# Kernel optimization log

Measured on AMD Instinct MI355X. Metric: run time of the kernel, lower is better.

Reference implementation:

```python
import jax, jax.numpy as jnp
import numpy as np

# Model dims (match init_kwargs)
B, H_HIST, L, C = 2, 7, 256, 512
H = H_HIST + 1          # dialogue turns after concatenating current utterance
N_HEADS = 8
N_TOP = 4               # window_size
D_HEAD = C // N_HEADS


def setup_inputs() -> dict:
    key = jax.random.key(0)
    ks = jax.random.split(key, 12)
    s = 0.02
    return {
        "global_attn_map": jax.random.normal(ks[0], (B, H, H), jnp.float32),
        "history_context": jax.random.normal(ks[1], (B, H_HIST, L, C), jnp.float32),
        "current_context": jax.random.normal(ks[2], (B, L, C), jnp.float32),
        "h_context_mask": jnp.ones((B, H_HIST, L), jnp.bool_),
        "c_context_mask": jnp.ones((B, L), jnp.bool_),
        "history_mask": jnp.ones((B, H_HIST), jnp.bool_),
        # 3 experts stacked on leading axis: 0=self, 1=past, 2=future
        "Wq": s * jax.random.normal(ks[3], (3, C, C), jnp.float32),
        "bq": jnp.zeros((3, C), jnp.float32),
        "Wk": s * jax.random.normal(ks[4], (3, C, C), jnp.float32),
        "bk": jnp.zeros((3, C), jnp.float32),
        "Wv": s * jax.random.normal(ks[5], (3, C, C), jnp.float32),
        "bv": jnp.zeros((3, C), jnp.float32),
        "Wo": s * jax.random.normal(ks[6], (3, C, C), jnp.float32),
        "bo": jnp.zeros((3, C), jnp.float32),
    }


def _mha(ctx, indx, Wq, bq, Wk, bk, Wv, bv, Wo, bo):
    """Cross-attention of every turn j (query) against its top-k gathered turns (key/value).
    ctx: (b,H,l,c), indx: (b,H,K) indices into the turn axis. Returns (b,H,K,l,c)."""
    b, Ht, l, c = ctx.shape
    K = indx.shape[-1]
    scale = 1.0 / np.sqrt(D_HEAD)
    q = (ctx @ Wq + bq).reshape(b, Ht, l, N_HEADS, D_HEAD)
    k = (ctx @ Wk + bk).reshape(b, Ht, l, N_HEADS, D_HEAD)
    v = (ctx @ Wv + bv).reshape(b, Ht, l, N_HEADS, D_HEAD)
    bidx = jnp.arange(b)[:, None, None]
    kg = k[bidx, indx]          # (b,H,K,l,nh,d)  gather KV turns
    vg = v[bidx, indx]
    scores = jnp.einsum('bhind,bhkjnd->bhknij', q, kg) * scale   # (b,H,K,nh,l,l)
    attn = jax.nn.softmax(scores, axis=-1)
    out = jnp.einsum('bhknij,bhkjnd->bhkind', attn, vg).reshape(b, Ht, K, l, c)
    return out @ Wo + bo


def _wise(ctx, attn_map, indx, Wq, bq, Wk, bk, Wv, bv, Wo, bo):
    """Vectorized form of the triple python loop: for each (batch, turn j, slot k) pick
    self/past/future expert by comparing j with indx[b,j,k], then combine weighted by attn_map."""
    outs = [_mha(ctx, indx, Wq[e], bq[e], Wk[e], bk[e], Wv[e], bv[e], Wo[e], bo[e])
            for e in range(3)]  # each (b,H,K,l,c); 0=self,1=past,2=future
    j = jnp.arange(ctx.shape[1])[None, :, None]
    sel_self = (indx == j)[..., None, None]
    sel_future = (indx > j)[..., None, None]
    combined = jnp.where(sel_self, outs[0], jnp.where(sel_future, outs[2], outs[1]))
    return jnp.einsum('bhk,bhklc->bhlc', attn_map, combined)


def reference(global_attn_map, history_context, current_context,
              h_context_mask, c_context_mask, history_mask,
              Wq, bq, Wk, bk, Wv, bv, Wo, bo):
    ctx = jnp.concatenate([history_context, current_context[:, None]], axis=1)  # (b,H,l,c)
    val, indx = jax.lax.top_k(global_attn_map, N_TOP)   # (b,H,K)
    n_attn = jax.nn.softmax(val, axis=-1)
    w = (Wq, bq, Wk, bk, Wv, bv, Wo, bo)
    h = jax.nn.relu(_wise(ctx, n_attn, indx, *w)) + ctx
    h = jax.nn.relu(_wise(h, n_attn, indx, *w)) + h
    return h
```

## Files before the change

kernel.cpp:

```cpp
#include <hip/hip_runtime.h>
#include <hip/hip_bf16.h>

constexpr int B   = 2;
constexpr int HH  = 7;
constexpr int H   = 8;
constexpr int L   = 256;
constexpr int C   = 512;
constexpr int NH  = 8;
constexpr int DH  = 64;
constexpr int KS  = 4;
constexpr int BH  = B * H;
constexpr int M4  = B * H * L;
constexpr size_t S = (size_t)B * H * L * C;

typedef __attribute__((ext_vector_type(8))) short short8;
typedef __attribute__((ext_vector_type(4))) float f32x4;
typedef unsigned short u16;
typedef unsigned int u32;

__device__ inline float bf2f(u16 u) {
    u32 x = ((u32)u) << 16;
    return __uint_as_float(x);
}
__device__ inline u16 f2bf(float f) {
    __hip_bfloat16 h = __float2bfloat16(f);
    return *reinterpret_cast<u16*>(&h);
}
__device__ inline u32 packbf(float lo, float hi) {
    return ((u32)f2bf(hi) << 16) | (u32)f2bf(lo);
}
__device__ inline void gload16(const void* g, void* l) {
    __builtin_amdgcn_global_load_lds(
        (const __attribute__((address_space(1))) void*)g,
        (__attribute__((address_space(3))) void*)l,
        16, 0, 0);
}
__device__ inline void vmcnt0() {
    asm volatile("s_waitcnt vmcnt(0)" ::: "memory");
}
__device__ inline void vmcnt4() {
    asm volatile("s_waitcnt vmcnt(4)" ::: "memory");
}

__global__ __launch_bounds__(256) void concat_cast_kernel(
    const float* __restrict__ hist, const float* __restrict__ cur,
    float* __restrict__ ctx, u16* __restrict__ Xb)
{
    size_t i4 = (size_t)blockIdx.x * 256 + threadIdx.x;
    size_t elem = i4 * 4;
    int c  = (int)(elem & (C - 1));
    size_t rest = elem >> 9;
    int l  = (int)(rest & (L - 1));
    int bh = (int)(rest >> 8);
    int h  = bh & (H - 1);
    int b  = bh >> 3;
    float4 v;
    if (h < HH) {
        size_t off = ((((size_t)b * HH + h) * L + l) * C + c);
        v = *reinterpret_cast<const float4*>(hist + off);
    } else {
        size_t off = (((size_t)b * L + l) * C + c);
        v = *reinterpret_cast<const float4*>(cur + off);
    }
    *reinterpret_cast<float4*>(ctx + elem) = v;
    ushort4 o;
    o.x = f2bf(v.x); o.y = f2bf(v.y); o.z = f2bf(v.z); o.w = f2bf(v.w);
    *reinterpret_cast<ushort4*>(Xb + elem) = o;
}

__global__ void topk_kernel(const float* __restrict__ gmap,
                            float* __restrict__ attnw,
                            int* __restrict__ indxO,
                            int* __restrict__ expertO)
{
    int t = threadIdx.x;
    if (t >= BH) return;
    int h = t & (H - 1);
    const float* row = gmap + (size_t)t * H;
    float v[H];
    #pragma unroll
    for (int j = 0; j < H; ++j) v[j] = row[j];
    float sel[KS]; int si[KS];
    #pragma unroll
    for (int kk = 0; kk < KS; ++kk) {
        float best = -1e30f; int bi = 0;
        #pragma unroll
        for (int j = 0; j < H; ++j) {
            if (v[j] > best) { best = v[j]; bi = j; }
        }
        sel[kk] = best; si[kk] = bi; v[bi] = -1e30f;
    }
    float mx = sel[0];
    float w[KS]; float sum = 0.f;
    #pragma unroll
    for (int kk = 0; kk < KS; ++kk) { w[kk] = __expf(sel[kk] - mx); sum += w[kk]; }
    float inv = 1.f / sum;
    #pragma unroll
    for (int kk = 0; kk < KS; ++kk) {
        attnw[t * KS + kk] = w[kk] * inv;
        indxO[t * KS + kk] = si[kk];
        int e = (si[kk] == h) ? 0 : ((si[kk] > h) ? 2 : 1);
        expertO[t * KS + kk] = e;
    }
}

__global__ __launch_bounds__(256) void biasc_kernel(
    const float* __restrict__ bo,
    const float* __restrict__ attnw, const int* __restrict__ expertArr,
    float* __restrict__ biasC)
{
    int bh = blockIdx.x;
    float a[KS]; int e[KS];
    #pragma unroll
    for (int k = 0; k < KS; ++k) {
        a[k] = attnw[bh * KS + k];
        e[k] = expertArr[bh * KS + k];
    }
    #pragma unroll
    for (int it = 0; it < 2; ++it) {
        int c = threadIdx.x + it * 256;
        float s = 0.f;
        #pragma unroll
        for (int k = 0; k < KS; ++k)
            s += a[k] * bo[(size_t)e[k] * C + c];
        biasC[(size_t)bh * C + c] = s;
    }
}

__global__ __launch_bounds__(256) void cast_w_kernel(
    const float* __restrict__ Wq, const float* __restrict__ Wk,
    const float* __restrict__ Wv, u16* __restrict__ Wt)
{
    int p = blockIdx.z;
    int e = p / 3, t = p % 3;
    const float* W = (t == 0 ? Wq : (t == 1 ? Wk : Wv)) + (size_t)e * C * C;
    __shared__ float tile[32][33];
    int k0 = blockIdx.y * 32, n0 = blockIdx.x * 32;
    int tc = threadIdx.x & 31, tr = threadIdx.x >> 5;
    #pragma unroll
    for (int i = 0; i < 4; ++i) {
        int r = tr + i * 8;
        tile[r][tc] = W[(size_t)(k0 + r) * C + n0 + tc];
    }
    __syncthreads();
    #pragma unroll
    for (int i = 0; i < 4; ++i) {
        int r = tr + i * 8;
        Wt[(size_t)p * C * C + (size_t)(n0 + r) * C + k0 + tc] = f2bf(tile[tc][r]);
    }
}

__global__ __launch_bounds__(256) void cast_wo_kernel(
    const float* __restrict__ Wo, u16* __restrict__ Wot)
{
    int p = blockIdx.z;
    const float* W = Wo + (size_t)p * C * C;
    __shared__ float tile[32][33];
    int k0 = blockIdx.y * 32, n0 = blockIdx.x * 32;
    int tc = threadIdx.x & 31, tr = threadIdx.x >> 5;
    #pragma unroll
    for (int i = 0; i < 4; ++i) {
        int r = tr + i * 8;
        tile[r][tc] = W[(size_t)(k0 + r) * C + n0 + tc];
    }
    __syncthreads();
    #pragma unroll
    for (int i = 0; i < 4; ++i) {
        int r = tr + i * 8;
        Wot[(size_t)p * C * C + (size_t)(n0 + r) * C + k0 + tc] = f2bf(tile[tc][r]);
    }
}

__global__ __launch_bounds__(256) void proj_mfma(
    const u16* __restrict__ Xb, const u16* __restrict__ Wt,
    const float* __restrict__ bq, const float* __restrict__ bk,
    const float* __restrict__ bv,
    u16* __restrict__ out)
{
    constexpr int BK = 32;
    constexpr int NT = C / BK;
    int p = blockIdx.z;
    int e = p / 3, t = p % 3;
    const float* bias = (t == 0 ? bq : (t == 1 ? bk : bv)) + (size_t)e * C;
    u16* Y = out + (size_t)p * S;
    const u16* Wp = Wt + (size_t)p * C * C;

    int m0 = blockIdx.y * 128;
    int n0 = blockIdx.x * 128;

    __shared__ u16 As[2][128 * BK];
    __shared__ u16 Bs[2][128 * BK];

    int tid  = threadIdx.x;
    int lane = tid & 63;
    int wid  = tid >> 6;
    int wr = wid >> 1, wc = wid & 1;
    int c = lane & 15, gl = lane >> 4;

    f32x4 acc[4][4];
    #pragma unroll
    for (int n = 0; n < 4; ++n)
        #pragma unroll
        for (int m = 0; m < 4; ++m)
            acc[n][m] = (f32x4){0.f, 0.f, 0.f, 0.f};

    int rowA = wr * 64 + c;
    int rowB = wc * 64 + c;

    auto stage = [&](int bb, int kt) {
        int k0 = kt * BK;
        #pragma unroll
        for (int it = 0; it < 2; ++it) {
            int base = it * 256 + wid * 64;
            int ch = base + lane;
            int r = ch >> 2, s = ch & 3;
            int r_src = r ^ ((r >> 2) & 1);
            int s_src = s ^ (r_src & 3);
            gload16(Xb + (size_t)(m0 + r_src) * C + k0 + s_src * 8,
                    &As[bb][base * 8]);
        }
        #pragma unroll
        for (int it = 0; it < 2; ++it) {
            int base = it * 256 + wid * 64;
            int ch = base + lane;
            int r = ch >> 2, s = ch & 3;
            int r_src = r ^ ((r >> 2) & 1);
            int s_src = s ^ (r_src & 3);
            gload16(Wp + (size_t)(n0 + r_src) * C + k0 + s_src * 8,
                    &Bs[bb][base * 8]);
        }
    };

    stage(0, 0);

    for (int kt = 0; kt < NT; ++kt) {
        int bb = kt & 1;
        if (kt + 1 < NT) {
            stage(bb ^ 1, kt + 1);
            vmcnt4();
        } else {
            vmcnt0();
        }
        __syncthreads();
        const char* Ab = (const char*)&As[bb][0];
        const char* Bb = (const char*)&Bs[bb][0];
        short8 af[4], bfr[4];
        #pragma unroll
        for (int m = 0; m < 4; ++m) {
            int row = rowA + m * 16;
            af[m] = *reinterpret_cast<const short8*>(
                Ab + ((row * 64 + gl * 16) ^ ((row & 7) << 4)));
        }
        #pragma unroll
        for (int n = 0; n < 4; ++n) {
            int row = rowB + n * 16;
            bfr[n] = *reinterpret_cast<const short8*>(
                Bb + ((row * 64 + gl * 16) ^ ((row & 7) << 4)));
        }
        #pragma unroll
        for (int n = 0; n < 4; ++n)
            #pragma unroll
            for (int m = 0; m < 4; ++m)
                acc[n][m] = __builtin_amdgcn_mfma_f32_16x16x32_bf16(
                    bfr[n], af[m], acc[n][m], 0, 0, 0);
        if (kt + 1 < NT) __syncthreads();
    }

    int mrow = m0 + wr * 64 + c;
    int colb = n0 + wc * 64 + gl * 4;
    #pragma unroll
    for (int n = 0; n < 4; ++n) {
        int col = colb + n * 16;
        float4 b4 = *reinterpret_cast<const float4*>(&bias[col]);
        #pragma unroll
        for (int m = 0; m < 4; ++m) {
            int row = mrow + m * 16;
            uint2 v;
            v.x = packbf(acc[n][m][0] + b4.x, acc[n][m][1] + b4.y);
            v.y = packbf(acc[n][m][2] + b4.z, acc[n][m][3] + b4.w);
            *reinterpret_cast<uint2*>(&Y[(size_t)row * C + col]) = v;
        }
    }
}

__global__ __launch_bounds__(256) void attn_mfma(
    const u16* __restrict__ qkv,
    const int* __restrict__ indx, const int* __restrict__ expertArr,
    const float* __restrict__ attnw,
    u16* __restrict__ Obuf)
{
    int head = blockIdx.x;
    int slot = blockIdx.y;
    int z    = blockIdx.z;
    int bh   = z >> 1, qh = z & 1;
    int b    = bh >> 3;
    int mi   = bh * KS + slot;
    int src  = indx[mi];
    int e    = expertArr[mi];
    float ak = attnw[mi];
    int qbase = qh * 128;

    const u16* qp = qkv + (size_t)(e * 3 + 0) * S + (size_t)bh * L * C + head * DH;
    const u16* kp = qkv + (size_t)(e * 3 + 1) * S + (size_t)(b * H + src) * L * C + head * DH;
    const u16* vp = qkv + (size_t)(e * 3 + 2) * S + (size_t)(b * H + src) * L * C + head * DH;

    __shared__ u16 Ks[64 * 64];
    __shared__ u16 Vt[64 * 64];
    __shared__ u16 Pl[4][32 * 64];

    int tid = threadIdx.x, lane = tid & 63, w = tid >> 6;
    int c = lane & 15, gl = lane >> 4;
    int qoff = qbase + w * 32;

    short8 qf[2][2];
    #pragma unroll
    for (int n = 0; n < 2; ++n)
        #pragma unroll
        for (int kf = 0; kf < 2; ++kf)
            qf[n][kf] = *reinterpret_cast<const short8*>(
                qp + (size_t)(qoff + n * 16 + c) * C + kf * 32 + 8 * gl);

    f32x4 accO[4][2];
    #pragma unroll
    for (int m = 0; m < 4; ++m)
        #pragma unroll
        for (int n = 0; n < 2; ++n)
            accO[m][n] = (f32x4){0.f, 0.f, 0.f, 0.f};
    float mrun[2], lrun[2];
    #pragma unroll
    for (int n = 0; n < 2; ++n) { mrun[n] = -1e30f; lrun[n] = 0.f; }

    char* Plw = (char*)&Pl[w][0];

    for (int t = 0; t < 4; ++t) {
        int c0 = t * 64;
        __syncthreads();
        #pragma unroll
        for (int it = 0; it < 2; ++it) {
            int ch = tid + 256 * it;
            int r = ch >> 3, cb = ch & 7;
            short8 kv = *reinterpret_cast<const short8*>(kp + (size_t)(c0 + r) * C + cb * 8);
            int ad = (r * 128 + cb * 16) ^ ((r & 7) << 4);
            *reinterpret_cast<short8*>((char*)Ks + ad) = kv;
        }
        {
            int rp = tid & 31;
            int d0 = (tid >> 5) * 8;
            const u16* v0p = vp + (size_t)(c0 + 2 * rp) * C + d0;
            const u16* v1p = v0p + C;
            ushort4 a0 = *reinterpret_cast<const ushort4*>(v0p);
            ushort4 a1 = *reinterpret_cast<const ushort4*>(v0p + 4);
            ushort4 b0 = *reinterpret_cast<const ushort4*>(v1p);
            ushort4 b1 = *reinterpret_cast<const ushort4*>(v1p + 4);
            u16 va[8] = {a0.x, a0.y, a0.z, a0.w, a1.x, a1.y, a1.z, a1.w};
            u16 vb[8] = {b0.x, b0.y, b0.z, b0.w, b1.x, b1.y, b1.z, b1.w};
            #pragma unroll
            for (int j = 0; j < 8; ++j) {
                u32 pk = ((u32)vb[j] << 16) | (u32)va[j];
                int ad = ((d0 + j) * 128 + rp * 4) ^ (((d0 + j) & 7) << 4);
                *reinterpret_cast<u32*>((char*)Vt + ad) = pk;
            }
        }
        __syncthreads();

        f32x4 accS[4][2];
        #pragma unroll
        for (int m = 0; m < 4; ++m)
            #pragma unroll
            for (int n = 0; n < 2; ++n)
                accS[m][n] = (f32x4){0.f, 0.f, 0.f, 0.f};
        #pragma unroll
        for (int kf = 0; kf < 2; ++kf) {
            short8 ka[4];
            #pragma unroll
            for (int m = 0; m < 4; ++m) {
                int row = m * 16 + c;
                ka[m] = *reinterpret_cast<const short8*>(
                    (char*)Ks + ((row * 128 + (kf * 32 + 8 * gl) * 2) ^ ((row & 7) << 4)));
            }
            #pragma unroll
            for (int m = 0; m < 4; ++m)
                #pragma unroll
                for (int n = 0; n < 2; ++n)
                    accS[m][n] = __builtin_amdgcn_mfma_f32_16x16x32_bf16(
                        ka[m], qf[n][kf], accS[m][n], 0, 0, 0);
        }

        #pragma unroll
        for (int n = 0; n < 2; ++n) {
            float tm = -1e30f;
            #pragma unroll
            for (int m = 0; m < 4; ++m)
                #pragma unroll
                for (int r = 0; r < 4; ++r)
                    tm = fmaxf(tm, accS[m][n][r] * 0.125f);
            tm = fmaxf(tm, __shfl_xor(tm, 16));
            tm = fmaxf(tm, __shfl_xor(tm, 32));
            float nm = fmaxf(mrun[n], tm);
            float al = __expf(mrun[n] - nm);
            mrun[n] = nm;
            lrun[n] *= al;
            #pragma unroll
            for (int m = 0; m < 4; ++m)
                #pragma unroll
                for (int r = 0; r < 4; ++r)
                    accO[m][n][r] *= al;
            float ps = 0.f;
            #pragma unroll
            for (int m = 0; m < 4; ++m)
                #pragma unroll
                for (int r = 0; r < 4; ++r) {
                    float pv = __expf(accS[m][n][r] * 0.125f - nm);
                    accS[m][n][r] = pv;
                    ps += pv;
                }
            lrun[n] += ps;
            int row = n * 16 + c;
            int sw = (row & 7) << 4;
            #pragma unroll
            for (int m = 0; m < 4; ++m) {
                u32 p0 = packbf(accS[m][n][0], accS[m][n][1]);
                u32 p1 = packbf(accS[m][n][2], accS[m][n][3]);
                int base = row * 128 + (m * 16 + 4 * gl) * 2;
                *reinterpret_cast<u32*>(Plw + (base ^ sw)) = p0;
                *reinterpret_cast<u32*>(Plw + ((base + 4) ^ sw)) = p1;
            }
        }

        #pragma unroll
        for (int kf = 0; kf < 2; ++kf) {
            short8 va[4], pb[2];
            #pragma unroll
            for (int m = 0; m < 4; ++m) {
                int row = m * 16 + c;
                va[m] = *reinterpret_cast<const short8*>(
                    (char*)Vt + ((row * 128 + (kf * 32 + 8 * gl) * 2) ^ ((row & 7) << 4)));
            }
            #pragma unroll
            for (int n = 0; n < 2; ++n) {
                int row = n * 16 + c;
                pb[n] = *reinterpret_cast<const short8*>(
                    Plw + ((row * 128 + (kf * 32 + 8 * gl) * 2) ^ ((row & 7) << 4)));
            }
            #pragma unroll
            for (int m = 0; m < 4; ++m)
                #pragma unroll
                for (int n = 0; n < 2; ++n)
                    accO[m][n] = __builtin_amdgcn_mfma_f32_16x16x32_bf16(
                        va[m], pb[n], accO[m][n], 0, 0, 0);
        }
    }

    float inv[2];
    #pragma unroll
    for (int n = 0; n < 2; ++n) {
        float lv = lrun[n];
        lv += __shfl_xor(lv, 16);
        lv += __shfl_xor(lv, 32);
        inv[n] = ak / lv;
    }
    #pragma unroll
    for (int m = 0; m < 4; ++m)
        #pragma unroll
        for (int n = 0; n < 2; ++n) {
            int row = n * 16 + c;
            int sw = (row & 7) << 4;
            float o0 = accO[m][n][0] * inv[n];
            float o1 = accO[m][n][1] * inv[n];
            float o2 = accO[m][n][2] * inv[n];
            float o3 = accO[m][n][3] * inv[n];
            int base = row * 128 + (m * 16 + 4 * gl) * 2;
            *reinterpret_cast<u32*>(Plw + (base ^ sw)) = packbf(o0, o1);
            *reinterpret_cast<u32*>(Plw + ((base + 4) ^ sw)) = packbf(o2, o3);
        }
    #pragma unroll
    for (int it = 0; it < 4; ++it) {
        int q = it * 8 + (lane >> 3), cb = lane & 7;
        short8 ov = *reinterpret_cast<const short8*>(
            Plw + ((q * 128 + cb * 16) ^ ((q & 7) << 4)));
        *reinterpret_cast<short8*>(
            Obuf + ((size_t)mi * L + qoff + q) * C + head * DH + cb * 8) = ov;
    }
}

__global__ __launch_bounds__(256) void wo_fused_ew(
    const u16* __restrict__ Obuf, const u16* __restrict__ Wot,
    const int* __restrict__ expertArr, const float* __restrict__ biasC,
    const float* __restrict__ xin,
    float* __restrict__ xout, u16* __restrict__ XbOut)
{
    constexpr int BK = 64;
    int bid  = blockIdx.x;
    int xcd  = bid & 7;
    int slot = bid >> 3;
    int gwi  = xcd * 64 + slot;
    int bh   = gwi >> 5;
    int wp   = gwi & 31;
    int n0   = (wp & 7) * 64;
    int m0   = (wp >> 3) * 64;

    int e4[KS];
    #pragma unroll
    for (int k = 0; k < KS; ++k) e4[k] = expertArr[bh * KS + k];

    __shared__ u16 As[2][64 * BK];
    __shared__ u16 Bs[2][64 * BK];

    int tid = threadIdx.x, lane = tid & 63, wid = tid >> 6;
    int wr = wid >> 1, wc = wid & 1;
    int c = lane & 15, gl = lane >> 4;

    f32x4 acc[2][2];
    #pragma unroll
    for (int n = 0; n < 2; ++n)
        #pragma unroll
        for (int m = 0; m < 2; ++m)
            acc[n][m] = (f32x4){0.f, 0.f, 0.f, 0.f};

    auto stage = [&](int bb, int kt) {
        int kslot = kt >> 3;
        int k0    = (kt & 7) * BK;
        const u16* Ap = Obuf + ((size_t)(bh * KS + kslot) * L + m0) * C + k0;
        const u16* Bp = Wot + (size_t)e4[kslot] * C * C + (size_t)n0 * C + k0;
        #pragma unroll
        for (int it = 0; it < 2; ++it) {
            int base = wid * 64 + it * 256;
            int ch = base + lane;
            int r = ch >> 3, cb = ch & 7;
            int ksw = (cb ^ (r & 7)) << 3;
            gload16(Ap + (size_t)r * C + ksw, &As[bb][base * 8]);
        }
        #pragma unroll
        for (int it = 0; it < 2; ++it) {
            int base = wid * 64 + it * 256;
            int ch = base + lane;
            int r = ch >> 3, cb = ch & 7;
            int ksw = (cb ^ (r & 7)) << 3;
            gload16(Bp + (size_t)r * C + ksw, &Bs[bb][base * 8]);
        }
    };

    stage(0, 0);

    constexpr int NT = 4 * (C / BK);
    for (int kt = 0; kt < NT; ++kt) {
        int bb = kt & 1;
        if (kt + 1 < NT) {
            stage(bb ^ 1, kt + 1);
            vmcnt4();
        } else {
            vmcnt0();
        }
        __syncthreads();
        const char* Ab = (const char*)&As[bb][0];
        const char* Bb = (const char*)&Bs[bb][0];
        #pragma unroll
        for (int ks = 0; ks < 2; ++ks) {
            int kb2 = (ks * 32 + 8 * gl) * 2;
            short8 af[2], bfr[2];
            #pragma unroll
            for (int m = 0; m < 2; ++m) {
                int row = wr * 32 + m * 16 + c;
                af[m] = *reinterpret_cast<const short8*>(
                    Ab + ((row * 128 + kb2) ^ ((row & 7) << 4)));
            }
            #pragma unroll
            for (int n = 0; n < 2; ++n) {
                int row = wc * 32 + n * 16 + c;
                bfr[n] = *reinterpret_cast<const short8*>(
                    Bb + ((row * 128 + kb2) ^ ((row & 7) << 4)));
            }
            #pragma unroll
            for (int n = 0; n < 2; ++n)
                #pragma unroll
                for (int m = 0; m < 2; ++m)
                    acc[n][m] = __builtin_amdgcn_mfma_f32_16x16x32_bf16(
                        bfr[n], af[m], acc[n][m], 0, 0, 0);
        }
        if (kt + 1 < NT) __syncthreads();
    }

    const float* xr = xin + (size_t)bh * L * C;
    float* xo = xout + (size_t)bh * L * C;
    u16*   xb = XbOut + (size_t)bh * L * C;
    int mrow = m0 + wr * 32 + c;
    int colb = n0 + wc * 32 + gl * 4;
    #pragma unroll
    for (int n = 0; n < 2; ++n) {
        int col = colb + n * 16;
        float4 b4 = *reinterpret_cast<const float4*>(&biasC[(size_t)bh * C + col]);
        #pragma unroll
        for (int m = 0; m < 2; ++m) {
            int row = mrow + m * 16;
            float4 x4 = *reinterpret_cast<const float4*>(&xr[(size_t)row * C + col]);
            float o0 = fmaxf(acc[n][m][0] + b4.x, 0.f) + x4.x;
            float o1 = fmaxf(acc[n][m][1] + b4.y, 0.f) + x4.y;
            float o2 = fmaxf(acc[n][m][2] + b4.z, 0.f) + x4.z;
            float o3 = fmaxf(acc[n][m][3] + b4.w, 0.f) + x4.w;
            float4 ov; ov.x = o0; ov.y = o1; ov.z = o2; ov.w = o3;
            *reinterpret_cast<float4*>(&xo[(size_t)row * C + col]) = ov;
            uint2 pv;
            pv.x = packbf(o0, o1);
            pv.y = packbf(o2, o3);
            *reinterpret_cast<uint2*>(&xb[(size_t)row * C + col]) = pv;
        }
    }
}

extern "C" void kernel_launch(void* const* d_in, const int* in_sizes, int n_in,
                              void* d_out, int out_size, void* d_ws, size_t ws_size,
                              hipStream_t stream) {
    const float* gmap = (const float*)d_in[0];
    const float* hist = (const float*)d_in[1];
    const float* cur  = (const float*)d_in[2];
    const float* Wq   = (const float*)d_in[6];
    const float* bq   = (const float*)d_in[7];
    const float* Wk   = (const float*)d_in[8];
    const float* bk   = (const float*)d_in[9];
    const float* Wv   = (const float*)d_in[10];
    const float* bv   = (const float*)d_in[11];
    const float* Wo   = (const float*)d_in[12];
    const float* bo   = (const float*)d_in[13];
    float* outp       = (float*)d_out;

    char* ws = (char*)d_ws;
    float* ctx  = (float*)(ws);
    float* x1   = (float*)(ws + 4 * S);
    u16*   qkv  = (u16*)(ws + 12 * S);
    u16*   Obuf = (u16*)(ws + 30 * S);
    char*  tail = ws + 38 * S;
    float* attnw  = (float*)(tail);
    int*   indx   = (int*)(tail + 256);
    int*   expert = (int*)(tail + 512);
    float* biasC  = (float*)(tail + 1024);
    u16*   Wot    = (u16*)(tail + 64 * 1024);
    u16*   Xb     = (u16*)(tail + 2 * 1024 * 1024);
    u16*   Wt     = (u16*)(tail + 8 * 1024 * 1024);

    dim3 projGrid(C / 128, M4 / 128, 9);
    dim3 castWGrid(C / 32, C / 32, 9);
    dim3 castWoGrid(C / 32, C / 32, 3);
    dim3 attnGrid(NH, KS, BH * 2);
    int woBlocks = (C / 64) * (L / 64) * BH;
    int ewBlocks = (int)(S / 4 / 256);

    concat_cast_kernel<<<ewBlocks, 256, 0, stream>>>(hist, cur, ctx, Xb);
    topk_kernel<<<1, 64, 0, stream>>>(gmap, attnw, indx, expert);
    biasc_kernel<<<BH, 256, 0, stream>>>(bo, attnw, expert, biasC);
    cast_wo_kernel<<<castWoGrid, 256, 0, stream>>>(Wo, Wot);
    cast_w_kernel<<<castWGrid, 256, 0, stream>>>(Wq, Wk, Wv, Wt);

    proj_mfma<<<projGrid, 256, 0, stream>>>(Xb, Wt, bq, bk, bv, qkv);
    attn_mfma<<<attnGrid, 256, 0, stream>>>(qkv, indx, expert, attnw, Obuf);
    wo_fused_ew<<<woBlocks, 256, 0, stream>>>(Obuf, Wot, expert, biasC, ctx, x1, Xb);

    proj_mfma<<<projGrid, 256, 0, stream>>>(Xb, Wt, bq, bk, bv, qkv);
    attn_mfma<<<attnGrid, 256, 0, stream>>>(qkv, indx, expert, attnw, Obuf);
    wo_fused_ew<<<woBlocks, 256, 0, stream>>>(Obuf, Wot, expert, biasC, x1, outp, Xb);
}
```

Before: 180.8 us.

## Triple-buffer LDS staging in projection GEMMs and transpose output-GEMM epilogue layout

Both the QKV projection GEMM and the output-projection GEMM move from double to triple-buffered LDS staging. Each iteration now prefetches two k-tiles ahead and waits with vmcnt(8), so more global-to-LDS latency is hidden. The output GEMM also swaps its MFMA operand order, which changes the accumulator layout so the epilogue writes scalar elements (one column per lane) instead of float4/uint2 vectors. The cost is more shared memory per block, which may lower occupancy, and the scalar epilogue stores may coalesce worse than the vector stores.

```diff
diff --git a/kernel.cpp b/kernel.cpp
--- a/kernel.cpp
+++ b/kernel.cpp
@@ -35,12 +35,9 @@
         (__attribute__((address_space(3))) void*)l,
         16, 0, 0);
 }
-__device__ inline void vmcnt0() {
-    asm volatile("s_waitcnt vmcnt(0)" ::: "memory");
-}
-__device__ inline void vmcnt4() {
-    asm volatile("s_waitcnt vmcnt(4)" ::: "memory");
-}
+__device__ inline void vmcnt0() { asm volatile("s_waitcnt vmcnt(0)" ::: "memory"); }
+__device__ inline void vmcnt4() { asm volatile("s_waitcnt vmcnt(4)" ::: "memory"); }
+__device__ inline void vmcnt8() { asm volatile("s_waitcnt vmcnt(8)" ::: "memory"); }
 
 __global__ __launch_bounds__(256) void concat_cast_kernel(
     const float* __restrict__ hist, const float* __restrict__ cur,
@@ -188,8 +185,8 @@
     int m0 = blockIdx.y * 128;
     int n0 = blockIdx.x * 128;
 
-    __shared__ u16 As[2][128 * BK];
-    __shared__ u16 Bs[2][128 * BK];
+    __shared__ u16 As[3][128 * BK];
+    __shared__ u16 Bs[3][128 * BK];
 
     int tid  = threadIdx.x;
     int lane = tid & 63;
@@ -232,11 +229,15 @@
     };
 
     stage(0, 0);
-
+    stage(1, 1);
+
+    int bb = 0;
     for (int kt = 0; kt < NT; ++kt) {
-        int bb = kt & 1;
-        if (kt + 1 < NT) {
-            stage(bb ^ 1, kt + 1);
+        if (kt + 2 < NT) {
+            int s2 = bb + 2 >= 3 ? bb - 1 : bb + 2;
+            stage(s2, kt + 2);
+            vmcnt8();
+        } else if (kt + 1 < NT) {
             vmcnt4();
         } else {
             vmcnt0();
@@ -264,6 +265,7 @@
                 acc[n][m] = __builtin_amdgcn_mfma_f32_16x16x32_bf16(
                     bfr[n], af[m], acc[n][m], 0, 0, 0);
         if (kt + 1 < NT) __syncthreads();
+        bb = bb + 1 >= 3 ? 0 : bb + 1;
     }
 
     int mrow = m0 + wr * 64 + c;
@@ -503,8 +505,8 @@
     #pragma unroll
     for (int k = 0; k < KS; ++k) e4[k] = expertArr[bh * KS + k];
 
-    __shared__ u16 As[2][64 * BK];
-    __shared__ u16 Bs[2][64 * BK];
+    __shared__ u16 As[3][64 * BK];
+    __shared__ u16 Bs[3][64 * BK];
 
     int tid = threadIdx.x, lane = tid & 63, wid = tid >> 6;
     int wr = wid >> 1, wc = wid & 1;
@@ -512,10 +514,10 @@
 
     f32x4 acc[2][2];
     #pragma unroll
-    for (int n = 0; n < 2; ++n)
-        #pragma unroll
-        for (int m = 0; m < 2; ++m)
-            acc[n][m] = (f32x4){0.f, 0.f, 0.f, 0.f};
+    for (int m = 0; m < 2; ++m)
+        #pragma unroll
+        for (int n = 0; n < 2; ++n)
+            acc[m][n] = (f32x4){0.f, 0.f, 0.f, 0.f};
 
     auto stage = [&](int bb, int kt) {
         int kslot = kt >> 3;
@@ -541,12 +543,16 @@
     };
 
     stage(0, 0);
+    stage(1, 1);
 
     constexpr int NT = 4 * (C / BK);
+    int bb = 0;
     for (int kt = 0; kt < NT; ++kt) {
-        int bb = kt & 1;
-        if (kt + 1 < NT) {
-            stage(bb ^ 1, kt + 1);
+        if (kt + 2 < NT) {
+            int s2 = bb + 2 >= 3 ? bb - 1 : bb + 2;
+            stage(s2, kt + 2);
+            vmcnt8();
+        } else if (kt + 1 < NT) {
             vmcnt4();
         } else {
             vmcnt0();
@@ -571,38 +577,36 @@
                     Bb + ((row * 128 + kb2) ^ ((row & 7) << 4)));
             }
             #pragma unroll
-            for (int n = 0; n < 2; ++n)
+            for (int m = 0; m < 2; ++m)
                 #pragma unroll
-                for (int m = 0; m < 2; ++m)
-                    acc[n][m] = __builtin_amdgcn_mfma_f32_16x16x32_bf16(
-                        bfr[n], af[m], acc[n][m], 0, 0, 0);
+                for (int n = 0; n < 2; ++n)
+                    acc[m][n] = __builtin_amdgcn_mfma_f32_16x16x32_bf16(
+                        af[m], bfr[n], acc[m][n], 0, 0, 0);
         }
         if (kt + 1 < NT) __syncthreads();
+        bb = bb + 1 >= 3 ? 0 : bb + 1;
     }
 
     const float* xr = xin + (size_t)bh * L * C;
     float* xo = xout + (size_t)bh * L * C;
     u16*   xb = XbOut + (size_t)bh * L * C;
-    int mrow = m0 + wr * 32 + c;
-    int colb = n0 + wc * 32 + gl * 4;
-    #pragma unroll
-    for (int n = 0; n < 2; ++n) {
-        int col = colb + n * 16;
-        float4 b4 = *reinterpret_cast<const float4*>(&biasC[(size_t)bh * C + col]);
-        #pragma unroll
-        for (int m = 0; m < 2; ++m) {
-            int row = mrow + m * 16;
-            float4 x4 = *reinterpret_cast<const float4*>(&xr[(size_t)row * C + col]);
-            float o0 = fmaxf(acc[n][m][0] + b4.x, 0.f) + x4.x;
-            float o1 = fmaxf(acc[n][m][1] + b4.y, 0.f) + x4.y;
-            float o2 = fmaxf(acc[n][m][2] + b4.z, 0.f) + x4.z;
-            float o3 = fmaxf(acc[n][m][3] + b4.w, 0.f) + x4.w;
-            float4 ov; ov.x = o0; ov.y = o1; ov.z = o2; ov.w = o3;
-            *reinterpret_cast<float4*>(&xo[(size_t)row * C + col]) = ov;
-            uint2 pv;
-            pv.x = packbf(o0, o1);
-            pv.y = packbf(o2, o3);
-            *reinterpret_cast<uint2*>(&xb[(size_t)row * C + col]) = pv;
+    float biasS[2];
+    #pragma unroll
+    for (int n = 0; n < 2; ++n)
+        biasS[n] = biasC[(size_t)bh * C + n0 + wc * 32 + n * 16 + c];
+    #pragma unroll
+    for (int m = 0; m < 2; ++m) {
+        #pragma unroll
+        for (int r = 0; r < 4; ++r) {
+            int row = m0 + wr * 32 + m * 16 + 4 * gl + r;
+            #pragma unroll
+            for (int n = 0; n < 2; ++n) {
+                int col = n0 + wc * 32 + n * 16 + c;
+                float v = acc[m][n][r] + biasS[n];
+                float o = fmaxf(v, 0.f) + xr[(size_t)row * C + col];
+                xo[(size_t)row * C + col] = o;
+                xb[(size_t)row * C + col] = f2bf(o);
+            }
         }
     }
 }
```

Result: no change. 179.1 us (-0.9%).
